# Performance work log

Measured on AMD Instinct MI355X. Metric: run time of the kernel, lower is better.

The kernel has to match this reference:

```python
import jax, jax.numpy as jnp
import numpy as np

N_NODES = 100000
N_EDGES = 1000000
IN_DIM = 64
HID = 64
N_CLUSTER = 30
REG = 0.01


def glorot(key, shape):
    lim = np.sqrt(6.0 / (shape[0] + shape[1]))
    return jax.random.uniform(key, shape, jnp.float32, -lim, lim)


def setup_inputs() -> dict:
    key = jax.random.key(0)
    k1, k2, k3, k4, k5 = jax.random.split(key, 5)
    x = jax.random.normal(k1, (N_NODES, IN_DIM), jnp.float32)
    edge_index = jax.random.randint(k2, (2, N_EDGES), 0, N_NODES, jnp.int64)
    edge_attr = jax.random.uniform(k3, (N_EDGES,), jnp.float32)
    W1 = glorot(k4, (IN_DIM, HID))
    b1 = jnp.zeros((HID,), jnp.float32)
    W2 = glorot(k5, (HID, N_CLUSTER))
    b2 = jnp.zeros((N_CLUSTER,), jnp.float32)
    return {"x": x, "edge_index": edge_index, "edge_attr": edge_attr,
            "W1": W1, "b1": b1, "W2": W2, "b2": b2}


def gcn_conv(x, W, b, src, dst, w):
    # PyG GCNConv with edge weights: add self-loops (weight 1), symmetric norm.
    h = x @ W  # [N, out]
    deg = jax.ops.segment_sum(w, dst, num_segments=N_NODES) + 1.0  # self-loop
    dinv = jax.lax.rsqrt(deg)
    norm = dinv[src] * w * dinv[dst]  # [E]
    agg = jax.ops.segment_sum(norm[:, None] * h[src], dst, num_segments=N_NODES)
    agg = agg + h / deg[:, None]  # self-loop contribution: norm = 1/deg
    return agg + b


def reference(x, edge_index, edge_attr, W1, b1, W2, b2):
    src, dst = edge_index[0], edge_index[1]
    h = jax.nn.relu(gcn_conv(x, W1, b1, src, dst, edge_attr))
    # dropout p=0 -> identity
    X2 = gcn_conv(h, W2, b2, src, dst, edge_attr)
    FX = jax.nn.softmax(X2, axis=-1)  # [N, C]
    FF = jnp.sum(FX[src] * FX[dst], axis=-1)  # [E]
    NFX = jnp.log(1.0 - FX ** 2)  # [N, C]
    preg = -jnp.sum(jnp.log(1.0001 - jnp.exp(jnp.sum(NFX, axis=0))))
    loss = jnp.mean((FF - edge_attr) ** 2)
    return FX, loss + REG * preg
```

## Files before the change

### kernel.cpp

```cpp
#include <hip/hip_runtime.h>
#include <hip/hip_fp16.h>
#include <math.h>

#define N_NODES 100000
#define N_EDGES 1000000
#define IN_DIM 64
#define HID 64
#define NC 30
#define NCP 32
#define REG_C 0.01f

#define NTILES (N_NODES / 16)
#define NBUCK 391
#define EPB_A 2048
#define NBLK_A 489
#define GEMM_BLOCKS 512

typedef _Float16 half8 __attribute__((ext_vector_type(8)));
typedef float f32x4 __attribute__((ext_vector_type(4)));

__device__ __forceinline__ unsigned char enc_fp8(float v) {
    return (unsigned char)(__builtin_amdgcn_cvt_pk_fp8_f32(v, v, 0, false) & 0xFF);
}
__device__ __forceinline__ float dec_fp8(unsigned char b) {
    return __builtin_amdgcn_cvt_f32_fp8((int)b, 0);
}
__device__ __forceinline__ float dot4_fp8(unsigned a, unsigned b) {
    float s = __builtin_amdgcn_cvt_f32_fp8((int)a, 0) * __builtin_amdgcn_cvt_f32_fp8((int)b, 0);
    s += __builtin_amdgcn_cvt_f32_fp8((int)a, 1) * __builtin_amdgcn_cvt_f32_fp8((int)b, 1);
    s += __builtin_amdgcn_cvt_f32_fp8((int)a, 2) * __builtin_amdgcn_cvt_f32_fp8((int)b, 2);
    s += __builtin_amdgcn_cvt_f32_fp8((int)a, 3) * __builtin_amdgcn_cvt_f32_fp8((int)b, 3);
    return s;
}

__global__ void hist_gemm(const int* __restrict__ dst, int* __restrict__ histT,
                          const float* __restrict__ X, const float* __restrict__ W,
                          unsigned char* __restrict__ H8) {
    if (blockIdx.x < NBLK_A) {
        __shared__ int cnt[NBUCK];
        for (int i = threadIdx.x; i < NBUCK; i += 256) cnt[i] = 0;
        __syncthreads();
        int e0 = blockIdx.x * EPB_A;
#pragma unroll
        for (int j = 0; j < 8; ++j) {
            int e = e0 + j * 256 + threadIdx.x;
            if (e < N_EDGES) atomicAdd(&cnt[dst[e] >> 8], 1);
        }
        __syncthreads();
        for (int b = threadIdx.x; b < NBUCK; b += 256)
            histT[b * NBLK_A + blockIdx.x] = cnt[b];
        return;
    }
    const int lane = threadIdx.x & 63;
    const int wave = threadIdx.x >> 6;
    const int qd = lane >> 4;
    const int l = lane & 15;
    half8 bfrag[2][4];
#pragma unroll
    for (int kb = 0; kb < 2; ++kb)
#pragma unroll
        for (int t = 0; t < 4; ++t)
#pragma unroll
            for (int j = 0; j < 8; ++j)
                bfrag[kb][t][j] = (_Float16)W[(kb * 32 + qd * 8 + j) * 64 + t * 16 + l];

    const int gb = blockIdx.x - NBLK_A;
    const int waveStride = GEMM_BLOCKS * 4;
    for (int ntile = gb * 4 + wave; ntile < NTILES; ntile += waveStride) {
        const int node0 = ntile * 16;
        const float* arow = X + (size_t)(node0 + l) * 64 + qd * 8;
        half8 af0, af1;
#pragma unroll
        for (int j = 0; j < 8; ++j) {
            af0[j] = (_Float16)arow[j];
            af1[j] = (_Float16)arow[32 + j];
        }
        f32x4 acc[4];
#pragma unroll
        for (int t = 0; t < 4; ++t) acc[t] = (f32x4){0.f, 0.f, 0.f, 0.f};
#pragma unroll
        for (int t = 0; t < 4; ++t) {
            acc[t] = __builtin_amdgcn_mfma_f32_16x16x32_f16(af0, bfrag[0][t], acc[t], 0, 0, 0);
            acc[t] = __builtin_amdgcn_mfma_f32_16x16x32_f16(af1, bfrag[1][t], acc[t], 0, 0, 0);
        }
#pragma unroll
        for (int t = 0; t < 4; ++t)
#pragma unroll
            for (int rr = 0; rr < 4; ++rr)
                H8[(size_t)(node0 + qd * 4 + rr) * 64 + t * 16 + l] = enc_fp8(acc[t][rr]);
    }
}

__global__ void scanA(int* __restrict__ histT, int* __restrict__ bucketTotal) {
    __shared__ int s[NBLK_A];
    int b = blockIdx.x;
    for (int i = threadIdx.x; i < NBLK_A; i += 256) s[i] = histT[b * NBLK_A + i];
    __syncthreads();
    if (threadIdx.x == 0) {
        int run = 0;
        for (int i = 0; i < NBLK_A; ++i) { int t = s[i]; s[i] = run; run += t; }
        bucketTotal[b] = run;
    }
    __syncthreads();
    for (int i = threadIdx.x; i < NBLK_A; i += 256) histT[b * NBLK_A + i] = s[i];
}

__global__ void scanB(const int* __restrict__ bucketTotal, int* __restrict__ bucketBase) {
    __shared__ int s[NBUCK];
    for (int i = threadIdx.x; i < NBUCK; i += 256) s[i] = bucketTotal[i];
    __syncthreads();
    if (threadIdx.x == 0) {
        int run = 0;
        for (int i = 0; i < NBUCK; ++i) { int t = s[i]; s[i] = run; run += t; }
    }
    __syncthreads();
    for (int i = threadIdx.x; i < NBUCK; i += 256) bucketBase[i] = s[i];
    if (threadIdx.x == 0) bucketBase[NBUCK] = N_EDGES;
}

__global__ void scatter_coarse(const int* __restrict__ src, const int* __restrict__ dst,
                               const float* __restrict__ w, const int* __restrict__ histT,
                               const int* __restrict__ bucketBase,
                               int2* __restrict__ sw, unsigned char* __restrict__ dl) {
    __shared__ int cur[NBUCK];
    int bl = blockIdx.x;
    for (int b = threadIdx.x; b < NBUCK; b += 256)
        cur[b] = bucketBase[b] + histT[b * NBLK_A + bl];
    __syncthreads();
    int e0 = bl * EPB_A;
#pragma unroll
    for (int j = 0; j < 8; ++j) {
        int e = e0 + j * 256 + threadIdx.x;
        if (e < N_EDGES) {
            int d = dst[e];
            int pos = atomicAdd(&cur[d >> 8], 1);
            sw[pos] = make_int2(src[e], __float_as_int(w[e]));
            dl[pos] = (unsigned char)(d & 255);
        }
    }
}

__global__ void bucket_deg(const int2* __restrict__ sw, const unsigned char* __restrict__ dl,
                           const int* __restrict__ bucketBase, float* __restrict__ dinv,
                           float* __restrict__ invdeg, int* __restrict__ rowptr) {
    __shared__ int cnt[256];
    __shared__ float degf[256];
    __shared__ int sc[256];
    int b = blockIdx.x, tid = threadIdx.x;
    cnt[tid] = 0; degf[tid] = 0.f;
    __syncthreads();
    int p0 = bucketBase[b], p1 = bucketBase[b + 1];
    for (int p = p0 + tid; p < p1; p += 256) {
        int d = dl[p];
        atomicAdd(&cnt[d], 1);
        atomicAdd(&degf[d], __int_as_float(sw[p].y));
    }
    __syncthreads();
    sc[tid] = cnt[tid];
    __syncthreads();
    for (int off = 1; off < 256; off <<= 1) {
        int t = (tid >= off) ? sc[tid - off] : 0;
        __syncthreads();
        sc[tid] += t;
        __syncthreads();
    }
    int node = b * 256 + tid;
    if (node < N_NODES) {
        float d = degf[tid] + 1.0f;
        dinv[node] = rsqrtf(d);
        invdeg[node] = 1.0f / d;
        rowptr[node] = p0 + sc[tid] - cnt[tid];
    }
    if (b == 0 && tid == 0) rowptr[N_NODES] = N_EDGES;
}

__global__ void bucket_scatter(const int2* __restrict__ sw, const unsigned char* __restrict__ dl,
                               const int* __restrict__ bucketBase, const int* __restrict__ rowptr,
                               const float* __restrict__ dinv,
                               int2* __restrict__ edata2, int2* __restrict__ wd) {
    __shared__ int cur[256];
    __shared__ float ldinv[256];
    int b = blockIdx.x, tid = threadIdx.x;
    int node = b * 256 + tid;
    if (node < N_NODES) { cur[tid] = rowptr[node]; ldinv[tid] = dinv[node]; }
    __syncthreads();
    int p0 = bucketBase[b], p1 = bucketBase[b + 1];
    for (int p = p0 + tid; p < p1; p += 256) {
        int d = dl[p];
        int2 r = sw[p];
        float wv = __int_as_float(r.y);
        float norm = dinv[r.x] * wv * ldinv[d];
        int pos = atomicAdd(&cur[d], 1);
        edata2[pos] = make_int2(r.x, __float_as_int(norm));
        wd[pos] = make_int2(r.y, b * 256 + d);
    }
}

__global__ void agg64_fused(const int* __restrict__ rowptr, const int2* __restrict__ edata2,
                            const unsigned char* __restrict__ H8, const float* __restrict__ invdeg,
                            const float* __restrict__ b1, _Float16* __restrict__ h2h) {
    int node = blockIdx.x * 4 + (threadIdx.x >> 6);
    int lane = threadIdx.x & 63;
    if (node >= N_NODES) return;
    int p = rowptr[node], end = rowptr[node + 1];
    float a0 = 0.f, a1 = 0.f, a2 = 0.f, a3 = 0.f;
    float a4 = 0.f, a5 = 0.f, a6 = 0.f, a7 = 0.f;
    for (; p + 7 < end; p += 8) {
        int2 e0 = edata2[p],     e1 = edata2[p + 1], e2 = edata2[p + 2], e3 = edata2[p + 3];
        int2 e4 = edata2[p + 4], e5 = edata2[p + 5], e6 = edata2[p + 6], e7 = edata2[p + 7];
        a0 += __int_as_float(e0.y) * dec_fp8(H8[(size_t)e0.x * 64 + lane]);
        a1 += __int_as_float(e1.y) * dec_fp8(H8[(size_t)e1.x * 64 + lane]);
        a2 += __int_as_float(e2.y) * dec_fp8(H8[(size_t)e2.x * 64 + lane]);
        a3 += __int_as_float(e3.y) * dec_fp8(H8[(size_t)e3.x * 64 + lane]);
        a4 += __int_as_float(e4.y) * dec_fp8(H8[(size_t)e4.x * 64 + lane]);
        a5 += __int_as_float(e5.y) * dec_fp8(H8[(size_t)e5.x * 64 + lane]);
        a6 += __int_as_float(e6.y) * dec_fp8(H8[(size_t)e6.x * 64 + lane]);
        a7 += __int_as_float(e7.y) * dec_fp8(H8[(size_t)e7.x * 64 + lane]);
    }
    for (; p + 1 < end; p += 2) {
        int2 e0 = edata2[p], e1 = edata2[p + 1];
        a0 += __int_as_float(e0.y) * dec_fp8(H8[(size_t)e0.x * 64 + lane]);
        a1 += __int_as_float(e1.y) * dec_fp8(H8[(size_t)e1.x * 64 + lane]);
    }
    if (p < end) {
        int2 e0 = edata2[p];
        a0 += __int_as_float(e0.y) * dec_fp8(H8[(size_t)e0.x * 64 + lane]);
    }
    float v = ((a0 + a1) + (a2 + a3)) + ((a4 + a5) + (a6 + a7)) +
              dec_fp8(H8[(size_t)node * 64 + lane]) * invdeg[node] + b1[lane];
    h2h[(size_t)node * 64 + lane] = (_Float16)fmaxf(v, 0.f);
}

__global__ void linear30(const _Float16* __restrict__ H, const float* __restrict__ W2,
                         __half* __restrict__ HH16) {
    __shared__ float sW[64 * NC];
    __shared__ float sH[8 * 64];
    for (int i = threadIdx.x; i < 64 * NC; i += blockDim.x) sW[i] = W2[i];
    int node0 = blockIdx.x * 8;
    for (int i = threadIdx.x; i < 8 * 64; i += blockDim.x) {
        int n = node0 + (i >> 6);
        sH[i] = (n < N_NODES) ? (float)H[(size_t)n * 64 + (i & 63)] : 0.f;
    }
    __syncthreads();
    int ln = threadIdx.x >> 5;
    int c = threadIdx.x & 31;
    int node = node0 + ln;
    if (node < N_NODES) {
        float acc = 0.f;
        if (c < NC) {
#pragma unroll
            for (int k = 0; k < 64; ++k) acc += sH[ln * 64 + k] * sW[k * NC + c];
        }
        HH16[(size_t)node * NCP + c] = __float2half(acc);
    }
}

__global__ void agg30_softmax_colsum(const int* __restrict__ rowptr, const int2* __restrict__ edata2,
                                     const __half* __restrict__ HH16,
                                     const float* __restrict__ invdeg,
                                     const float* __restrict__ b2, float* __restrict__ FX,
                                     unsigned char* __restrict__ FX8,
                                     float* __restrict__ colsum_part) {
    const int lane = threadIdx.x & 63;
    const int waveInBlock = threadIdx.x >> 6;
    const int half = lane >> 5;
    const int c = lane & 31;
    const bool activeC = (c < NC);
    const int wavesTotal = gridDim.x * (blockDim.x >> 6);
    const int w0 = blockIdx.x * (blockDim.x >> 6) + waveInBlock;

    const float bb = activeC ? b2[c] : 0.f;
    float lacc = 0.f;

    for (int pair = w0; pair < N_NODES / 2; pair += wavesTotal) {
        const int node = pair * 2 + half;
        int p = rowptr[node], end = rowptr[node + 1];
        float acc0 = 0.f, acc1 = 0.f, acc2 = 0.f, acc3 = 0.f;
        for (; p + 3 < end; p += 4) {
            int2 e0 = edata2[p],     e1 = edata2[p + 1];
            int2 e2 = edata2[p + 2], e3 = edata2[p + 3];
            acc0 += __int_as_float(e0.y) * __half2float(HH16[(size_t)e0.x * NCP + c]);
            acc1 += __int_as_float(e1.y) * __half2float(HH16[(size_t)e1.x * NCP + c]);
            acc2 += __int_as_float(e2.y) * __half2float(HH16[(size_t)e2.x * NCP + c]);
            acc3 += __int_as_float(e3.y) * __half2float(HH16[(size_t)e3.x * NCP + c]);
        }
        for (; p < end; ++p) {
            int2 e0 = edata2[p];
            acc0 += __int_as_float(e0.y) * __half2float(HH16[(size_t)e0.x * NCP + c]);
        }
        float selfv = __half2float(HH16[(size_t)node * NCP + c]);
        float x = activeC ? ((acc0 + acc1) + (acc2 + acc3) + selfv * invdeg[node] + bb)
                          : -INFINITY;
        float mx = x;
        for (int off = 16; off; off >>= 1) mx = fmaxf(mx, __shfl_xor(mx, off));
        float e = activeC ? expf(x - mx) : 0.f;
        float s = e;
        for (int off = 16; off; off >>= 1) s += __shfl_xor(s, off);
        float fx = e / s;
        if (activeC) {
            FX[(size_t)node * NC + c] = fx;
            FX8[(size_t)node * NCP + c] = enc_fp8(fx);
            lacc += log1pf(-fx * fx);
        } else {
            FX8[(size_t)node * NCP + c] = 0;
        }
    }
    lacc += __shfl_xor(lacc, 32);
    __shared__ float part[4][NC];
    if (half == 0 && activeC) part[waveInBlock][c] = lacc;
    __syncthreads();
    if (threadIdx.x < NC) {
        float v = part[0][threadIdx.x] + part[1][threadIdx.x] +
                  part[2][threadIdx.x] + part[3][threadIdx.x];
        atomicAdd(&colsum_part[(blockIdx.x & 63) * 32 + threadIdx.x], v);
    }
}

__global__ void edge_loss_sorted(const int2* __restrict__ edata2, const int2* __restrict__ wd,
                                 const unsigned char* __restrict__ FX8,
                                 float* __restrict__ mse_part) {
    int e = blockIdx.x * blockDim.x + threadIdx.x;
    float v = 0.f;
    if (e < N_EDGES) {
        int2 sn = edata2[e];
        int2 wdv = wd[e];
        const uint4* rs = (const uint4*)(FX8 + (size_t)sn.x * NCP);
        const uint4* rd = (const uint4*)(FX8 + (size_t)wdv.y * NCP);
        uint4 a0 = rs[0], a1 = rs[1];
        uint4 b0 = rd[0], b1 = rd[1];
        float ff = dot4_fp8(a0.x, b0.x) + dot4_fp8(a0.y, b0.y) +
                   dot4_fp8(a0.z, b0.z) + dot4_fp8(a0.w, b0.w) +
                   dot4_fp8(a1.x, b1.x) + dot4_fp8(a1.y, b1.y) +
                   dot4_fp8(a1.z, b1.z) + dot4_fp8(a1.w, b1.w);
        float diff = ff - __int_as_float(wdv.x);
        v = diff * diff;
    }
    for (int off = 32; off > 0; off >>= 1) v += __shfl_down(v, off);
    __shared__ float ps[4];
    int lane = threadIdx.x & 63, wv = threadIdx.x >> 6;
    if (lane == 0) ps[wv] = v;
    __syncthreads();
    if (threadIdx.x == 0)
        atomicAdd(&mse_part[blockIdx.x & 63], ps[0] + ps[1] + ps[2] + ps[3]);
}

__global__ void finalize(const float* __restrict__ colsum_part, const float* __restrict__ mse_part,
                         float* __restrict__ out_loss) {
    int t = threadIdx.x;
    float m = mse_part[t];
    for (int off = 32; off > 0; off >>= 1) m += __shfl_down(m, off);
    float term = 0.f;
    if (t < NC) {
        float s = 0.f;
        for (int k = 0; k < 64; ++k) s += colsum_part[k * 32 + t];
        term = logf(1.0001f - expf(s));
    }
    for (int off = 32; off > 0; off >>= 1) term += __shfl_down(term, off);
    if (t == 0)
        out_loss[0] = m / (float)N_EDGES - REG_C * term;
}

extern "C" void kernel_launch(void* const* d_in, const int* in_sizes, int n_in,
                              void* d_out, int out_size, void* d_ws, size_t ws_size,
                              hipStream_t stream) {
    const float* x  = (const float*)d_in[0];
    const int*   ei = (const int*)d_in[1];
    const float* ea = (const float*)d_in[2];
    const float* W1 = (const float*)d_in[3];
    const float* b1 = (const float*)d_in[4];
    const float* W2 = (const float*)d_in[5];
    const float* b2 = (const float*)d_in[6];
    const int* srcI = ei;
    const int* dstI = ei + N_EDGES;

    float* FX   = (float*)d_out;
    float* loss = FX + (size_t)N_NODES * NC;

    float* ws = (float*)d_ws;
    float*         dinv   = ws;
    float*         invdeg = ws + 100000;
    unsigned char* h8     = (unsigned char*)(ws + 200000);
    _Float16*      h2h    = (_Float16*)(ws + 1800000);
    __half*        hh16   = (__half*)(ws + 5000000);
    unsigned char* fx8    = (unsigned char*)(ws + 6600000);
    float*         colsum_part = ws + 7400000;
    float*         mse_part    = ws + 7402048;
    int*           rowptr = (int*)(ws + 7402112);
    int*           histT  = (int*)(ws + 7502114);
    int*           bucketTotal = (int*)(ws + 7693314);
    int*           bucketBase  = (int*)(ws + 7693706);
    int2*          sw     = (int2*)(ws + 7694098);
    unsigned char* dl     = (unsigned char*)(ws + 9694098);
    int2*          edata2 = (int2*)(ws + 9944098);
    int2*          wd     = (int2*)(ws + 11944098);

    hipMemsetAsync(colsum_part, 0, (2048 + 64) * sizeof(float), stream);

    hist_gemm<<<NBLK_A + GEMM_BLOCKS, 256, 0, stream>>>(dstI, histT, x, W1, h8);
    scanA<<<NBUCK, 256, 0, stream>>>(histT, bucketTotal);
    scanB<<<1, 256, 0, stream>>>(bucketTotal, bucketBase);
    scatter_coarse<<<NBLK_A, 256, 0, stream>>>(srcI, dstI, ea, histT, bucketBase, sw, dl);
    bucket_deg<<<NBUCK, 256, 0, stream>>>(sw, dl, bucketBase, dinv, invdeg, rowptr);
    bucket_scatter<<<NBUCK, 256, 0, stream>>>(sw, dl, bucketBase, rowptr, dinv, edata2, wd);
    agg64_fused<<<(N_NODES + 3) / 4, 256, 0, stream>>>(rowptr, edata2, h8, invdeg, b1, h2h);
    linear30<<<(N_NODES + 7) / 8, 256, 0, stream>>>(h2h, W2, hh16);
    agg30_softmax_colsum<<<4096, 256, 0, stream>>>(rowptr, edata2, hh16, invdeg, b2,
                                                   FX, fx8, colsum_part);
    edge_loss_sorted<<<(N_EDGES + 255) / 256, 256, 0, stream>>>(edata2, wd, fx8, mse_part);
    finalize<<<1, 64, 0, stream>>>(colsum_part, mse_part, loss);
}
```

Measured before the change: 303.0 us.

## Fuse layer-1 aggregation with second linear layer and fold memset into hist kernel

Each wave aggregates one node's 64-dim hidden row, applies ReLU into shared memory, and immediately computes the 30-wide projection with W2 staged in LDS. This removes the fp16 hidden-state round trip through global memory and one kernel launch. The colsum/mse zeroing moves into block 0 of the histogram kernel, dropping a separate memset call. The cost is that every block now reloads W2 (7.5 KB) into shared memory, and the matvec uses only 30 of 64 lanes per wave. The wave reads sH without a barrier, relying on same-wave lockstep execution.

```diff
diff --git a/kernel.cpp b/kernel.cpp
--- a/kernel.cpp
+++ b/kernel.cpp
@@ -35,8 +35,11 @@
 
 __global__ void hist_gemm(const int* __restrict__ dst, int* __restrict__ histT,
                           const float* __restrict__ X, const float* __restrict__ W,
-                          unsigned char* __restrict__ H8) {
+                          unsigned char* __restrict__ H8, float* __restrict__ zeroRegion) {
     if (blockIdx.x < NBLK_A) {
+        if (blockIdx.x == 0) {
+            for (int i = threadIdx.x; i < 2112; i += 256) zeroRegion[i] = 0.f;
+        }
         __shared__ int cnt[NBUCK];
         for (int i = threadIdx.x; i < NBUCK; i += 256) cnt[i] = 0;
         __syncthreads();
@@ -196,12 +199,18 @@
     }
 }
 
-__global__ void agg64_fused(const int* __restrict__ rowptr, const int2* __restrict__ edata2,
+__global__ void agg64_lin30(const int* __restrict__ rowptr, const int2* __restrict__ edata2,
                             const unsigned char* __restrict__ H8, const float* __restrict__ invdeg,
-                            const float* __restrict__ b1, _Float16* __restrict__ h2h) {
-    int node = blockIdx.x * 4 + (threadIdx.x >> 6);
+                            const float* __restrict__ b1, const float* __restrict__ W2,
+                            __half* __restrict__ HH16) {
+    __shared__ float sW[64 * NC];
+    __shared__ float sH[4][64];
+    for (int i = threadIdx.x; i < 64 * NC; i += 256) sW[i] = W2[i];
+    __syncthreads();
+
+    int wave = threadIdx.x >> 6;
     int lane = threadIdx.x & 63;
-    if (node >= N_NODES) return;
+    int node = blockIdx.x * 4 + wave;
     int p = rowptr[node], end = rowptr[node + 1];
     float a0 = 0.f, a1 = 0.f, a2 = 0.f, a3 = 0.f;
     float a4 = 0.f, a5 = 0.f, a6 = 0.f, a7 = 0.f;
@@ -228,30 +237,15 @@
     }
     float v = ((a0 + a1) + (a2 + a3)) + ((a4 + a5) + (a6 + a7)) +
               dec_fp8(H8[(size_t)node * 64 + lane]) * invdeg[node] + b1[lane];
-    h2h[(size_t)node * 64 + lane] = (_Float16)fmaxf(v, 0.f);
-}
-
-__global__ void linear30(const _Float16* __restrict__ H, const float* __restrict__ W2,
-                         __half* __restrict__ HH16) {
-    __shared__ float sW[64 * NC];
-    __shared__ float sH[8 * 64];
-    for (int i = threadIdx.x; i < 64 * NC; i += blockDim.x) sW[i] = W2[i];
-    int node0 = blockIdx.x * 8;
-    for (int i = threadIdx.x; i < 8 * 64; i += blockDim.x) {
-        int n = node0 + (i >> 6);
-        sH[i] = (n < N_NODES) ? (float)H[(size_t)n * 64 + (i & 63)] : 0.f;
-    }
-    __syncthreads();
-    int ln = threadIdx.x >> 5;
-    int c = threadIdx.x & 31;
-    int node = node0 + ln;
-    if (node < N_NODES) {
+    sH[wave][lane] = fmaxf(v, 0.f);
+
+    if (lane < NC) {
         float acc = 0.f;
-        if (c < NC) {
-#pragma unroll
-            for (int k = 0; k < 64; ++k) acc += sH[ln * 64 + k] * sW[k * NC + c];
-        }
-        HH16[(size_t)node * NCP + c] = __float2half(acc);
+#pragma unroll
+        for (int k = 0; k < 64; ++k) acc += sH[wave][k] * sW[k * NC + lane];
+        HH16[(size_t)node * NCP + lane] = __float2half(acc);
+    } else if (lane < NCP) {
+        HH16[(size_t)node * NCP + lane] = __float2half(0.f);
     }
 }
 
@@ -380,7 +374,6 @@
     float*         dinv   = ws;
     float*         invdeg = ws + 100000;
     unsigned char* h8     = (unsigned char*)(ws + 200000);
-    _Float16*      h2h    = (_Float16*)(ws + 1800000);
     __half*        hh16   = (__half*)(ws + 5000000);
     unsigned char* fx8    = (unsigned char*)(ws + 6600000);
     float*         colsum_part = ws + 7400000;
@@ -394,16 +387,13 @@
     int2*          edata2 = (int2*)(ws + 9944098);
     int2*          wd     = (int2*)(ws + 11944098);
 
-    hipMemsetAsync(colsum_part, 0, (2048 + 64) * sizeof(float), stream);
-
-    hist_gemm<<<NBLK_A + GEMM_BLOCKS, 256, 0, stream>>>(dstI, histT, x, W1, h8);
+    hist_gemm<<<NBLK_A + GEMM_BLOCKS, 256, 0, stream>>>(dstI, histT, x, W1, h8, colsum_part);
     scanA<<<NBUCK, 256, 0, stream>>>(histT, bucketTotal);
     scanB<<<1, 256, 0, stream>>>(bucketTotal, bucketBase);
     scatter_coarse<<<NBLK_A, 256, 0, stream>>>(srcI, dstI, ea, histT, bucketBase, sw, dl);
     bucket_deg<<<NBUCK, 256, 0, stream>>>(sw, dl, bucketBase, dinv, invdeg, rowptr);
     bucket_scatter<<<NBUCK, 256, 0, stream>>>(sw, dl, bucketBase, rowptr, dinv, edata2, wd);
-    agg64_fused<<<(N_NODES + 3) / 4, 256, 0, stream>>>(rowptr, edata2, h8, invdeg, b1, h2h);
-    linear30<<<(N_NODES + 7) / 8, 256, 0, stream>>>(h2h, W2, hh16);
+    agg64_lin30<<<N_NODES / 4, 256, 0, stream>>>(rowptr, edata2, h8, invdeg, b1, W2, hh16);
     agg30_softmax_colsum<<<4096, 256, 0, stream>>>(rowptr, edata2, hh16, invdeg, b2,
                                                    FX, fx8, colsum_part);
     edge_loss_sorted<<<(N_EDGES + 255) / 256, 256, 0, stream>>>(edata2, wd, fx8, mse_part);
```

After: 312.1 us. +3.0%, slower.
